# Kernel tuning notes

Hardware: AMD Instinct MI355X
Metric: run time of the kernel (lower is better)

Reference implementation:

```python
import jax, jax.numpy as jnp
import numpy as np

D_MODEL = 1024
NUM_HEADS = 16
D_FF = 2688
BATCH = 2
SEQ = 2048
EPS = 1e-5


def _trunc_normal(key, shape, std):
    # truncated normal on [-3, 3] then scaled by std (matches trunc_normal_(mean=0,std,a=-3,b=3) approximately)
    return std * jax.random.truncated_normal(key, -3.0 / std if std > 0 else -3.0, 3.0 / std if std > 0 else 3.0, shape, jnp.float32) * std / std if False else jax.random.truncated_normal(key, -3.0, 3.0, shape, jnp.float32) * std


def setup_inputs() -> dict:
    key = jax.random.key(0)
    ks = jax.random.split(key, 8)
    def lin(k, d_out, d_in):
        std = (2.0 / (d_in + d_out)) ** 0.5
        return _trunc_normal(k, (d_out, d_in), std)
    return {
        "x": jax.random.normal(ks[0], (BATCH, SEQ, D_MODEL), jnp.float32),
        "wqkv": lin(ks[1], 3 * D_MODEL, D_MODEL),
        "wo": lin(ks[2], D_MODEL, D_MODEL),
        "g1": jnp.ones((D_MODEL,), jnp.float32),
        "g2": jnp.ones((D_MODEL,), jnp.float32),
        "w1": lin(ks[3], D_FF, D_MODEL),
        "w2": lin(ks[4], D_MODEL, D_FF),
        "w3": lin(ks[5], D_FF, D_MODEL),
    }


def _rmsnorm(x, g):
    rms = jnp.sqrt(jnp.mean(x * x, axis=-1, keepdims=True) + EPS)
    return x * (g / rms)


def _mhsa(x, wqkv, wo):
    B, S, D = x.shape
    H, Dk = NUM_HEADS, D // NUM_HEADS
    qkv = jnp.einsum('bsd,ed->bse', x, wqkv)  # [B,S,3D]
    q, k, v = jnp.split(qkv, 3, axis=-1)
    def heads(t):
        return t.reshape(B, S, H, Dk).transpose(0, 2, 1, 3)  # [B,H,S,Dk]
    q, k, v = heads(q), heads(k), heads(v)
    scores = jnp.einsum('bhqd,bhkd->bhqk', q, k) / jnp.sqrt(jnp.asarray(Dk, x.dtype))
    causal = jnp.tril(jnp.ones((S, S), bool))
    scores = jnp.where(causal, scores, -jnp.inf)
    attn = jax.nn.softmax(scores, axis=-1)
    out = jnp.einsum('bhqk,bhkd->bhqd', attn, v)
    out = out.transpose(0, 2, 1, 3).reshape(B, S, D)
    return jnp.einsum('bsd,ed->bse', out, wo)


def _swiglu(x, w1, w2, w3):
    a = jnp.einsum('bsd,fd->bsf', x, w1)
    b = jnp.einsum('bsd,fd->bsf', x, w3)
    h = (a * jax.nn.sigmoid(a)) * b
    return jnp.einsum('bsf,df->bsd', h, w2)


def reference(x, wqkv, wo, g1, g2, w1, w2, w3):
    x = x + _mhsa(_rmsnorm(x, g1), wqkv, wo)
    x = x + _swiglu(_rmsnorm(x, g2), w1, w2, w3)
    return x
```

## Files before the change

kernel.cpp:

```cpp
#include <hip/hip_runtime.h>
#include <cstdint>
#include <cstddef>

typedef unsigned short u16;
typedef __attribute__((ext_vector_type(8))) short short8;
typedef __attribute__((ext_vector_type(4))) float float4v;

struct alignas(8) u16x4 { u16 x, y, z, w; };

__device__ __forceinline__ float bf2f(u16 u) {
  union { uint32_t i; float f; } x;
  x.i = ((uint32_t)u) << 16;
  return x.f;
}
__device__ __forceinline__ u16 f2bf(float f) {
  union { float f; uint32_t i; } x;
  x.f = f;
  uint32_t r = x.i + 0x7fffu + ((x.i >> 16) & 1u);
  return (u16)(r >> 16);
}
__device__ __forceinline__ int4 pack8(const float4& a, const float4& b) {
  int4 r;
  r.x = (uint32_t)f2bf(a.x) | ((uint32_t)f2bf(a.y) << 16);
  r.y = (uint32_t)f2bf(a.z) | ((uint32_t)f2bf(a.w) << 16);
  r.z = (uint32_t)f2bf(b.x) | ((uint32_t)f2bf(b.y) << 16);
  r.w = (uint32_t)f2bf(b.z) | ((uint32_t)f2bf(b.w) << 16);
  return r;
}

__device__ __forceinline__ void gload_lds16(const void* g, void* l) {
  __builtin_amdgcn_global_load_lds(
      (const __attribute__((address_space(1))) void*)g,
      (__attribute__((address_space(3))) void*)l, 16, 0, 0);
}

#define WAITV_BAR(N)                                              \
  do {                                                            \
    asm volatile("s_waitcnt vmcnt(%0)" ::"n"(N) : "memory");      \
    __builtin_amdgcn_s_barrier();                                 \
    __builtin_amdgcn_sched_barrier(0);                            \
  } while (0)

#define BAR_ONLY()                                                \
  do {                                                            \
    __builtin_amdgcn_sched_barrier(0);                            \
    __builtin_amdgcn_s_barrier();                                 \
    __builtin_amdgcn_sched_barrier(0);                            \
  } while (0)

__device__ __forceinline__ int2 xcd_swizzle_xmajor() {
  const int gx = gridDim.x, gy = gridDim.y;
  const int nwg = gx * gy;
  const int lin = blockIdx.x + blockIdx.y * gx;
  const int nl = (lin & 7) * (nwg >> 3) + (lin >> 3);
  const int bx = nl / gy;
  const int by = nl - bx * gy;
  return make_int2(bx, by);
}

struct PrepArgs {
  const float* src[5];
  u16* dst[5];
  int pre[6];
};

__global__ __launch_bounds__(256) void prep_kernel(PrepArgs a)
{
  const int g = blockIdx.x * 256 + threadIdx.x;
  if (g >= a.pre[5]) return;
  int t = 0;
#pragma unroll
  for (int i = 0; i < 5; i++) if (g >= a.pre[i + 1]) t = i + 1;
  const int idx = (g - a.pre[t]) * 8;
  const float* s = a.src[t] + idx;
  float4 v0 = *(const float4*)(s);
  float4 v1 = *(const float4*)(s + 4);
  *(int4*)(a.dst[t] + idx) = pack8(v0, v1);
}

template <int RMODE, bool OUTF32, int TN>
__global__ __launch_bounds__(256) void gemm_bt_kernel(
    const u16* __restrict__ A, const u16* __restrict__ B,
    void* __restrict__ Cv, const void* __restrict__ Rv,
    int M, int N, int K)
{
  constexpr int JN = TN / 32;
  constexpr int NLD = (TN == 128) ? 4 : 3;
  __shared__ u16 As[3][128 * 32];
  __shared__ u16 Bs[3][TN * 32];
  const int t = threadIdx.x;
  const int lane = t & 63;
  const int wave = t >> 6;
  const int l15 = lane & 15;
  const int quad = lane >> 4;
  const int wm = (wave >> 1) * 64;
  const int wn = (wave & 1) * (TN / 2);
  const int2 bb = xcd_swizzle_xmajor();
  const int m0 = bb.y * 128;
  const int n0 = bb.x * TN;
  const int sw = quad ^ ((l15 >> 1) & 3);

  float4v acc[4][JN] = {};

  const int r0 = t >> 2, q0s = (t & 3) ^ ((t >> 3) & 3);
  const int s1 = 256 + t;
  const int r1 = s1 >> 2, q1s = (s1 & 3) ^ ((s1 >> 3) & 3);

  auto stage = [&](int bi, int kk) {
    gload_lds16(A + (size_t)(m0 + r0) * K + kk + q0s * 8, &As[bi][(wave * 64) * 8]);
    gload_lds16(A + (size_t)(m0 + r1) * K + kk + q1s * 8, &As[bi][(256 + wave * 64) * 8]);
    gload_lds16(B + (size_t)(n0 + r0) * K + kk + q0s * 8, &Bs[bi][(wave * 64) * 8]);
    if (TN == 128)
      gload_lds16(B + (size_t)(n0 + r1) * K + kk + q1s * 8, &Bs[bi][(256 + wave * 64) * 8]);
  };
  auto compute = [&](int bi) {
    short8 af[4], bfr[JN];
#pragma unroll
    for (int i = 0; i < 4; i++)
      af[i] = *(const short8*)(&As[bi][((wm + i * 16 + l15) * 4 + sw) * 8]);
#pragma unroll
    for (int j = 0; j < JN; j++)
      bfr[j] = *(const short8*)(&Bs[bi][((wn + j * 16 + l15) * 4 + sw) * 8]);
#pragma unroll
    for (int i = 0; i < 4; i++)
#pragma unroll
      for (int j = 0; j < JN; j++)
        acc[i][j] = __builtin_amdgcn_mfma_f32_16x16x32_bf16(af[i], bfr[j], acc[i][j], 0, 0, 0);
  };

  const int nk = K >> 5;
  stage(0, 0);
  stage(1, 32);
  int bc = 0, bs = 2;
  for (int i = 0; i + 2 < nk; ++i) {
    stage(bs, (i + 2) << 5);
    WAITV_BAR(2 * NLD);
    compute(bc);
    BAR_ONLY();
    bc = (bc == 2) ? 0 : bc + 1;
    bs = (bs == 2) ? 0 : bs + 1;
  }
  WAITV_BAR(NLD);
  compute(bc);
  bc = (bc == 2) ? 0 : bc + 1;
  WAITV_BAR(0);
  compute(bc);

#pragma unroll
  for (int i = 0; i < 4; i++) {
#pragma unroll
    for (int r = 0; r < 4; r++) {
      const int row = m0 + wm + i * 16 + quad * 4 + r;
      const size_t base = (size_t)row * N;
#pragma unroll
      for (int j = 0; j < JN; j++) {
        const int col = n0 + wn + j * 16 + l15;
        float v = acc[i][j][r];
        if (RMODE == 1) v += ((const float*)Rv)[base + col];
        if (RMODE == 2) v += bf2f(((const u16*)Rv)[base + col]);
        if (OUTF32) ((float*)Cv)[base + col] = v;
        else        ((u16*)Cv)[base + col] = f2bf(v);
      }
    }
  }
}

__global__ __launch_bounds__(512) void gemm_w13_kernel(
    const u16* __restrict__ A, const u16* __restrict__ B1,
    const u16* __restrict__ B2, u16* __restrict__ C,
    int M, int N, int K)
{
  __shared__ u16 As[3][128 * 32];
  __shared__ u16 B1s[3][128 * 32];
  __shared__ u16 B2s[3][128 * 32];
  const int t = threadIdx.x;
  const int lane = t & 63;
  const int wave = t >> 6;
  const int l15 = lane & 15;
  const int quad = lane >> 4;
  const int wm = (wave >> 2) * 64;
  const int wn = (wave & 3) * 32;
  const int2 bb = xcd_swizzle_xmajor();
  const int m0 = bb.y * 128;
  const int n0 = bb.x * 128;
  const int sw = quad ^ ((l15 >> 1) & 3);

  float4v accA[4][2] = {};
  float4v accB[4][2] = {};

  const int r0 = t >> 2, q0s = (t & 3) ^ ((t >> 3) & 3);

  auto stage = [&](int bi, int kk) {
    gload_lds16(A  + (size_t)(m0 + r0) * K + kk + q0s * 8, &As[bi][(wave * 64) * 8]);
    gload_lds16(B1 + (size_t)(n0 + r0) * K + kk + q0s * 8, &B1s[bi][(wave * 64) * 8]);
    gload_lds16(B2 + (size_t)(n0 + r0) * K + kk + q0s * 8, &B2s[bi][(wave * 64) * 8]);
  };
  auto compute = [&](int bi) {
    short8 af[4], b1f[2], b2f[2];
#pragma unroll
    for (int i = 0; i < 4; i++)
      af[i] = *(const short8*)(&As[bi][((wm + i * 16 + l15) * 4 + sw) * 8]);
#pragma unroll
    for (int j = 0; j < 2; j++) {
      b1f[j] = *(const short8*)(&B1s[bi][((wn + j * 16 + l15) * 4 + sw) * 8]);
      b2f[j] = *(const short8*)(&B2s[bi][((wn + j * 16 + l15) * 4 + sw) * 8]);
    }
#pragma unroll
    for (int i = 0; i < 4; i++)
#pragma unroll
      for (int j = 0; j < 2; j++) {
        accA[i][j] = __builtin_amdgcn_mfma_f32_16x16x32_bf16(af[i], b1f[j], accA[i][j], 0, 0, 0);
        accB[i][j] = __builtin_amdgcn_mfma_f32_16x16x32_bf16(af[i], b2f[j], accB[i][j], 0, 0, 0);
      }
  };

  const int nk = K >> 5;
  stage(0, 0);
  stage(1, 32);
  int bc = 0, bs = 2;
  for (int i = 0; i + 2 < nk; ++i) {
    stage(bs, (i + 2) << 5);
    WAITV_BAR(6);
    compute(bc);
    BAR_ONLY();
    bc = (bc == 2) ? 0 : bc + 1;
    bs = (bs == 2) ? 0 : bs + 1;
  }
  WAITV_BAR(3);
  compute(bc);
  bc = (bc == 2) ? 0 : bc + 1;
  WAITV_BAR(0);
  compute(bc);

#pragma unroll
  for (int i = 0; i < 4; i++) {
#pragma unroll
    for (int r = 0; r < 4; r++) {
      const int row = m0 + wm + i * 16 + quad * 4 + r;
      const size_t base = (size_t)row * N;
#pragma unroll
      for (int j = 0; j < 2; j++) {
        const int col = n0 + wn + j * 16 + l15;
        float a = accA[i][j][r];
        float b = accB[i][j][r];
        float h = a / (1.f + __expf(-a)) * b;
        C[base + col] = f2bf(h);
      }
    }
  }
}

__global__ __launch_bounds__(256) void vtrans_kernel(
    const u16* __restrict__ qkv, u16* __restrict__ VtG)
{
  __shared__ u16 T[64 * 72];
  const int t = threadIdx.x;
  const int s0 = blockIdx.x * 64;
  const int bh = blockIdx.y, b = bh >> 4, h = bh & 15;
  {
    const int sl = t >> 2, dseg = (t & 3) * 16;
    const size_t src = ((size_t)b * 2048 + s0 + sl) * 3072 + 2048 + h * 64 + dseg;
    int4 v0 = *(const int4*)(qkv + src);
    int4 v1 = *(const int4*)(qkv + src + 8);
    *(int4*)(&T[sl * 72 + dseg]) = v0;
    *(int4*)(&T[sl * 72 + dseg + 8]) = v1;
  }
  __syncthreads();
  {
    const int d = t >> 2, sseg = (t & 3) * 16;
    alignas(16) u16 buf[16];
#pragma unroll
    for (int i = 0; i < 16; i++) buf[i] = T[(sseg + i) * 72 + d];
    u16* dst = VtG + ((size_t)bh * 64 + d) * 2048 + s0 + sseg;
    *(int4*)(dst) = *(const int4*)(&buf[0]);
    *(int4*)(dst + 8) = *(const int4*)(&buf[8]);
  }
}

__global__ __launch_bounds__(256) void attn_kernel(
    const u16* __restrict__ qkv, const u16* __restrict__ VtG,
    u16* __restrict__ outp)
{
  __shared__ u16 Ks[2][2][128 * 32];
  __shared__ u16 Vt[2][4][64 * 32];
  __shared__ u16 Pl[4][2048];
  const int t = threadIdx.x;
  const int lane = t & 63;
  const int wave = t >> 6;
  const int l15 = lane & 15;
  const int quad = lane >> 4;
  const int sw = quad ^ ((l15 >> 1) & 3);
  const int gx = gridDim.x;
  const int nwg = gx * gridDim.y;
  const int lin = blockIdx.x + blockIdx.y * gx;
  const int nl = (lin & 7) * (nwg >> 3) + (lin >> 3);
  const int bh = nl / gx;
  const int pair = nl - bh * gx;
  const int b = bh >> 4, h = bh & 15;
  const size_t srow = (size_t)b * 2048;
  const int rr = lane >> 2, qs = (lane & 3) ^ ((lane >> 3) & 3);
  u16* plw = Pl[wave];

  auto stageKV = [&](int bi, int ic) {
    const int c0 = ic * 128;
#pragma unroll
    for (int k = 0; k < 8; k++) {
      const int I = wave * 8 + k;
      if (I < 16) {
        const int half = I >> 3, rb = (I & 7) * 16, row = rb + rr;
        gload_lds16(qkv + (srow + c0 + row) * 3072 + 1024 + h * 64 + half * 32 + qs * 8,
                    &Ks[bi][half][rb * 32]);
      } else {
        const int g = (I - 16) >> 2, rb = ((I - 16) & 3) * 16, row = rb + rr;
        gload_lds16(VtG + ((size_t)bh * 64 + row) * 2048 + c0 + g * 32 + qs * 8,
                    &Vt[bi][g][rb * 32]);
      }
    }
  };

  for (int tsel = 0; tsel < 2; tsel++) {
    const int qt = tsel ? 31 - pair : pair;
    const int tq0 = qt * 64;
    const int q = tq0 + wave * 16 + l15;

    short8 qf[2];
    {
      const size_t qbase = (srow + q) * 3072 + h * 64;
#pragma unroll
      for (int dh = 0; dh < 2; dh++) {
        int4 raw = *(const int4*)(qkv + qbase + dh * 32 + quad * 8);
        const u16* rp = (const u16*)&raw;
        short8 f;
#pragma unroll
        for (int j = 0; j < 8; j++)
          ((u16*)&f)[j] = f2bf(bf2f(rp[j]) * 0.125f);
        qf[dh] = f;
      }
    }

    float m_i = -INFINITY, l_i = 0.f;
    float4v accO[4] = {};
    const int nc = (qt + 2) >> 1;

    stageKV(0, 0);
    for (int ic = 0; ic < nc; ic++) {
      const int cb = ic & 1;
      const int c0 = ic * 128;
      if (ic + 1 < nc) {
        stageKV(cb ^ 1, ic + 1);
        WAITV_BAR(8);
      } else {
        WAITV_BAR(0);
      }

      float4v accS[8];
#pragma unroll
      for (int ks = 0; ks < 8; ks++) {
        short8 kf0 = *(const short8*)(&Ks[cb][0][((ks * 16 + l15) * 4 + sw) * 8]);
        short8 kf1 = *(const short8*)(&Ks[cb][1][((ks * 16 + l15) * 4 + sw) * 8]);
        float4v z = {};
        z = __builtin_amdgcn_mfma_f32_16x16x32_bf16(kf0, qf[0], z, 0, 0, 0);
        accS[ks] = __builtin_amdgcn_mfma_f32_16x16x32_bf16(kf1, qf[1], z, 0, 0, 0);
      }

      if (ic == nc - 1) {
#pragma unroll
        for (int ks = 0; ks < 8; ks++)
#pragma unroll
          for (int r = 0; r < 4; r++)
            if (c0 + ks * 16 + quad * 4 + r > q) accS[ks][r] = -INFINITY;
      }

      float cmax = -INFINITY;
#pragma unroll
      for (int ks = 0; ks < 8; ks++)
#pragma unroll
        for (int r = 0; r < 4; r++) cmax = fmaxf(cmax, accS[ks][r]);
      cmax = fmaxf(cmax, __shfl_xor(cmax, 16));
      cmax = fmaxf(cmax, __shfl_xor(cmax, 32));
      const float mn = fmaxf(m_i, cmax);
      const float alpha = __expf(m_i - mn);

      float psum = 0.f;
#pragma unroll
      for (int ks = 0; ks < 8; ks++) {
        float p0 = __expf(accS[ks][0] - mn);
        float p1 = __expf(accS[ks][1] - mn);
        float p2 = __expf(accS[ks][2] - mn);
        float p3 = __expf(accS[ks][3] - mn);
        psum += (p0 + p1) + (p2 + p3);
        u16x4 pk;
        pk.x = f2bf(p0); pk.y = f2bf(p1); pk.z = f2bf(p2); pk.w = f2bf(p3);
        const int seg = ((ks & 1) * 2 + (quad >> 1)) ^ ((l15 >> 1) & 3);
        *(u16x4*)(&plw[(ks >> 1) * 512 + (l15 * 4 + seg) * 8 + (quad & 1) * 4]) = pk;
      }
      psum += __shfl_xor(psum, 16);
      psum += __shfl_xor(psum, 32);
      l_i = l_i * alpha + psum;
      m_i = mn;
#pragma unroll
      for (int ds = 0; ds < 4; ds++)
#pragma unroll
        for (int r = 0; r < 4; r++) accO[ds][r] *= alpha;

      __threadfence_block();

#pragma unroll
      for (int kh = 0; kh < 4; kh++) {
        short8 pf = *(const short8*)(&plw[kh * 512 + (l15 * 4 + sw) * 8]);
#pragma unroll
        for (int ds = 0; ds < 4; ds++) {
          short8 vf = *(const short8*)(&Vt[cb][kh][((ds * 16 + l15) * 4 + sw) * 8]);
          accO[ds] = __builtin_amdgcn_mfma_f32_16x16x32_bf16(vf, pf, accO[ds], 0, 0, 0);
        }
      }
      BAR_ONLY();
    }

    const float invl = 1.f / l_i;
    const size_t obase = (srow + q) * 1024 + h * 64;
#pragma unroll
    for (int ds = 0; ds < 4; ds++) {
      u16x4 pk;
      pk.x = f2bf(accO[ds][0] * invl);
      pk.y = f2bf(accO[ds][1] * invl);
      pk.z = f2bf(accO[ds][2] * invl);
      pk.w = f2bf(accO[ds][3] * invl);
      *(u16x4*)(outp + obase + ds * 16 + quad * 4) = pk;
    }
  }
}

template <bool XF32>
__global__ __launch_bounds__(256) void rmsnorm_kernel(
    const void* __restrict__ xv, const float* __restrict__ g, u16* __restrict__ o)
{
  const int row = blockIdx.x;
  const int t = threadIdx.x;
  float f0, f1, f2, f3;
  if (XF32) {
    float4 v = *(const float4*)((const float*)xv + (size_t)row * 1024 + t * 4);
    f0 = v.x; f1 = v.y; f2 = v.z; f3 = v.w;
  } else {
    int2 v = *(const int2*)((const u16*)xv + (size_t)row * 1024 + t * 4);
    const u16* p = (const u16*)&v;
    f0 = bf2f(p[0]); f1 = bf2f(p[1]); f2 = bf2f(p[2]); f3 = bf2f(p[3]);
  }
  float ss = f0 * f0 + f1 * f1 + f2 * f2 + f3 * f3;
#pragma unroll
  for (int off = 32; off > 0; off >>= 1) ss += __shfl_down(ss, off);
  __shared__ float red[4];
  if ((t & 63) == 0) red[t >> 6] = ss;
  __syncthreads();
  const float tot = red[0] + red[1] + red[2] + red[3];
  const float inv = rsqrtf(tot * (1.0f / 1024.0f) + 1e-5f);
  float4 gv = *(const float4*)(g + t * 4);
  u16x4 ov;
  ov.x = f2bf(f0 * gv.x * inv);
  ov.y = f2bf(f1 * gv.y * inv);
  ov.z = f2bf(f2 * gv.z * inv);
  ov.w = f2bf(f3 * gv.w * inv);
  *(u16x4*)(o + (size_t)row * 1024 + t * 4) = ov;
}

extern "C" void kernel_launch(void* const* d_in, const int* in_sizes, int n_in,
                              void* d_out, int out_size, void* d_ws, size_t ws_size,
                              hipStream_t stream)
{
  const float* x    = (const float*)d_in[0];
  const float* wqkv = (const float*)d_in[1];
  const float* wo   = (const float*)d_in[2];
  const float* g1   = (const float*)d_in[3];
  const float* g2   = (const float*)d_in[4];
  const float* w1   = (const float*)d_in[5];
  const float* w2   = (const float*)d_in[6];
  const float* w3   = (const float*)d_in[7];
  float* out = (float*)d_out;
  char* ws = (char*)d_ws;
  (void)in_sizes; (void)n_in; (void)out_size; (void)ws_size;

  size_t off = 0;
  auto alloc = [&](size_t bytes) { void* p = ws + off; off += (bytes + 255) & ~(size_t)255; return p; };
  u16* wqkvb = (u16*)alloc((size_t)3072 * 1024 * 2);
  u16* wob   = (u16*)alloc((size_t)1024 * 1024 * 2);
  u16* w1b   = (u16*)alloc((size_t)2688 * 1024 * 2);
  u16* w2b   = (u16*)alloc((size_t)2688 * 1024 * 2);
  u16* w3b   = (u16*)alloc((size_t)2688 * 1024 * 2);
  u16* S1    = (u16*)alloc((size_t)4096 * 1024 * 2);
  u16* S2    = (u16*)alloc((size_t)4096 * 3072 * 2);
  u16* S3    = (u16*)alloc((size_t)4096 * 1024 * 2);
  u16* VtG   = (u16*)alloc((size_t)32 * 64 * 2048 * 2);

  PrepArgs pa;
  const float* srcs[5] = {wqkv, wo, w1, w2, w3};
  u16* dsts[5] = {wqkvb, wob, w1b, w2b, w3b};
  const int nelem[5] = {3072 * 1024, 1024 * 1024, 2688 * 1024, 2688 * 1024, 2688 * 1024};
  int pre = 0;
  for (int i = 0; i < 5; i++) {
    pa.src[i] = srcs[i];
    pa.dst[i] = dsts[i];
    pa.pre[i] = pre;
    pre += nelem[i] / 8;
  }
  pa.pre[5] = pre;
  prep_kernel<<<(pre + 255) / 256, 256, 0, stream>>>(pa);

  rmsnorm_kernel<true><<<4096, 256, 0, stream>>>(x, g1, S1);
  gemm_bt_kernel<0, false, 128><<<dim3(24, 32), 256, 0, stream>>>(S1, wqkvb, S2,
                                                  nullptr, 4096, 3072, 1024);
  vtrans_kernel<<<dim3(32, 32), 256, 0, stream>>>(S2, VtG);
  attn_kernel<<<dim3(16, 32), 256, 0, stream>>>(S2, VtG, S1);
  gemm_bt_kernel<1, false, 64><<<dim3(16, 32), 256, 0, stream>>>(S1, wob, S3, x,
                                                  4096, 1024, 1024);
  rmsnorm_kernel<false><<<4096, 256, 0, stream>>>(S3, g2, S1);
  gemm_w13_kernel<<<dim3(21, 32), 512, 0, stream>>>(S1, w1b, w3b, S2,
                                                  4096, 2688, 1024);
  gemm_bt_kernel<2, true, 64><<<dim3(16, 32), 256, 0, stream>>>(S2, w2b, out, S3,
                                                  4096, 1024, 2688);
}
```

Baseline: 333.0 us.

## Split dual-GEMM SwiGLU main loop into two phases with interleaved loads and setprio

The fused W1/W3 GEMM loop is split into two phases. The first loads A and B1 fragments and runs the accA MFMAs, then the B2 tile is issued and the accB MFMAs run. Global-to-LDS issues and barriers are interleaved between the phases, and s_setprio raises wave priority around MFMA bursts, so memory traffic overlaps with compute at a finer grain. The cost is more barriers per k-step and wait counts that must be tuned by hand, which is easy to get wrong.

```diff
diff --git a/kernel.cpp b/kernel.cpp
--- a/kernel.cpp
+++ b/kernel.cpp
@@ -187,50 +187,72 @@
 
   float4v accA[4][2] = {};
   float4v accB[4][2] = {};
+  short8 af[4];
 
   const int r0 = t >> 2, q0s = (t & 3) ^ ((t >> 3) & 3);
 
-  auto stage = [&](int bi, int kk) {
+  auto issueAB1 = [&](int bi, int kk) {
     gload_lds16(A  + (size_t)(m0 + r0) * K + kk + q0s * 8, &As[bi][(wave * 64) * 8]);
     gload_lds16(B1 + (size_t)(n0 + r0) * K + kk + q0s * 8, &B1s[bi][(wave * 64) * 8]);
+  };
+  auto issueB2 = [&](int bi, int kk) {
     gload_lds16(B2 + (size_t)(n0 + r0) * K + kk + q0s * 8, &B2s[bi][(wave * 64) * 8]);
   };
-  auto compute = [&](int bi) {
-    short8 af[4], b1f[2], b2f[2];
+  auto ph1_core = [&](int bi) {
+    short8 b1f[2];
 #pragma unroll
     for (int i = 0; i < 4; i++)
       af[i] = *(const short8*)(&As[bi][((wm + i * 16 + l15) * 4 + sw) * 8]);
 #pragma unroll
-    for (int j = 0; j < 2; j++) {
+    for (int j = 0; j < 2; j++)
       b1f[j] = *(const short8*)(&B1s[bi][((wn + j * 16 + l15) * 4 + sw) * 8]);
+    __builtin_amdgcn_s_setprio(1);
+#pragma unroll
+    for (int i = 0; i < 4; i++)
+#pragma unroll
+      for (int j = 0; j < 2; j++)
+        accA[i][j] = __builtin_amdgcn_mfma_f32_16x16x32_bf16(af[i], b1f[j], accA[i][j], 0, 0, 0);
+    __builtin_amdgcn_s_setprio(0);
+  };
+  auto ph2_core = [&](int bi) {
+    short8 b2f[2];
+#pragma unroll
+    for (int j = 0; j < 2; j++)
       b2f[j] = *(const short8*)(&B2s[bi][((wn + j * 16 + l15) * 4 + sw) * 8]);
-    }
+    __builtin_amdgcn_s_setprio(1);
 #pragma unroll
     for (int i = 0; i < 4; i++)
 #pragma unroll
-      for (int j = 0; j < 2; j++) {
-        accA[i][j] = __builtin_amdgcn_mfma_f32_16x16x32_bf16(af[i], b1f[j], accA[i][j], 0, 0, 0);
+      for (int j = 0; j < 2; j++)
         accB[i][j] = __builtin_amdgcn_mfma_f32_16x16x32_bf16(af[i], b2f[j], accB[i][j], 0, 0, 0);
-      }
+    __builtin_amdgcn_s_setprio(0);
   };
 
   const int nk = K >> 5;
-  stage(0, 0);
-  stage(1, 32);
+  issueAB1(0, 0);  issueB2(0, 0);
+  issueAB1(1, 32); issueB2(1, 32);
+  WAITV_BAR(4);
+
   int bc = 0, bs = 2;
   for (int i = 0; i + 2 < nk; ++i) {
-    stage(bs, (i + 2) << 5);
-    WAITV_BAR(6);
-    compute(bc);
-    BAR_ONLY();
+    const int kk2 = (i + 2) << 5;
+    issueAB1(bs, kk2);
+    ph1_core(bc);
+    WAITV_BAR(5);
+    issueB2(bs, kk2);
+    ph2_core(bc);
+    WAITV_BAR(4);
     bc = (bc == 2) ? 0 : bc + 1;
     bs = (bs == 2) ? 0 : bs + 1;
   }
+  ph1_core(bc);
   WAITV_BAR(3);
-  compute(bc);
+  ph2_core(bc);
+  WAITV_BAR(1);
   bc = (bc == 2) ? 0 : bc + 1;
+  ph1_core(bc);
   WAITV_BAR(0);
-  compute(bc);
+  ph2_core(bc);
 
 #pragma unroll
   for (int i = 0; i < 4; i++) {
```

Result: slower. 342.0 us (+2.7%).
